# Kernel tuning notes

Hardware: AMD Instinct MI355X
Metric: run time of the kernel (lower is better)

## Reference

```python
import jax, jax.numpy as jnp
import numpy as np

# ---- fixed problem dimensions ----
B, S, T = 64, 200, 32          # batch of sequences, trees per seq, nodes per tree
V, E, C = 50000, 128, 128      # vocab, embedding_dim, encode_dim
H, OUT = 100, 104              # GRU hidden, output_dim
N = B * S * T                  # total nodes
D_MAX = 5                      # max depth of a 32-node complete binary tree


def setup_inputs() -> dict:
    key = jax.random.key(0)
    ks = jax.random.split(key, 16)
    # --- tree structure: every tree is a complete binary tree with T nodes ---
    local_parent = np.array([0] + [(i - 1) // 2 for i in range(1, T)], dtype=np.int64)
    local_depth = np.array([int(np.floor(np.log2(i + 1))) for i in range(T)], dtype=np.int64)
    num_trees = B * S
    offsets = np.arange(num_trees, dtype=np.int64) * T
    node_parent = (offsets[:, None] + local_parent[None, :]).reshape(-1)
    node_depth = np.tile(local_depth, num_trees)
    node_tree = np.repeat(np.arange(num_trees, dtype=np.int64), T)
    node_tokens = jax.random.randint(ks[0], (N,), 0, V, dtype=jnp.int64)
    sc = 0.05
    inp = {
        "node_tokens": node_tokens,
        "node_parent": jnp.asarray(node_parent),
        "node_tree": jnp.asarray(node_tree),
        "node_depth": jnp.asarray(node_depth),
        "emb": jax.random.normal(ks[1], (V, E), jnp.float32) * sc,
        "w_lin": jax.random.normal(ks[2], (C, E), jnp.float32) * sc,
        "b_lin": jnp.zeros((C,), jnp.float32),
        "w_ih_f": jax.random.normal(ks[3], (3 * H, C), jnp.float32) * sc,
        "w_hh_f": jax.random.normal(ks[4], (3 * H, H), jnp.float32) * sc,
        "b_ih_f": jnp.zeros((3 * H,), jnp.float32),
        "b_hh_f": jnp.zeros((3 * H,), jnp.float32),
        "w_ih_b": jax.random.normal(ks[5], (3 * H, C), jnp.float32) * sc,
        "w_hh_b": jax.random.normal(ks[6], (3 * H, H), jnp.float32) * sc,
        "b_ih_b": jnp.zeros((3 * H,), jnp.float32),
        "b_hh_b": jnp.zeros((3 * H,), jnp.float32),
        "fc_w": jax.random.normal(ks[7], (OUT, 2 * H), jnp.float32) * sc,
        "fc_b": jnp.zeros((OUT,), jnp.float32),
    }
    return inp


def _gru(x_sbc, w_ih, w_hh, b_ih, b_hh):
    """Torch-convention GRU over leading time axis. x_sbc: [S, B, C] -> [S, B, H]."""
    h0 = jnp.zeros((x_sbc.shape[1], w_hh.shape[1]), x_sbc.dtype)

    def step(h, xt):
        gx = xt @ w_ih.T + b_ih
        gh = h @ w_hh.T + b_hh
        xr, xz, xn = jnp.split(gx, 3, axis=-1)
        hr, hz, hn = jnp.split(gh, 3, axis=-1)
        r = jax.nn.sigmoid(xr + hr)
        z = jax.nn.sigmoid(xz + hz)
        n = jnp.tanh(xn + r * hn)
        h_new = (1.0 - z) * n + z * h
        return h_new, h_new

    _, hs = jax.lax.scan(step, h0, x_sbc)
    return hs


def reference(node_tokens, node_parent, node_tree, node_depth,
              emb, w_lin, b_lin,
              w_ih_f, w_hh_f, b_ih_f, b_hh_f,
              w_ih_b, w_hh_b, b_ih_b, b_hh_b,
              fc_w, fc_b):
    # per-node contribution: W * emb(token) + b   (recursion base of hidden_state)
    c = emb[node_tokens] @ w_lin.T + b_lin               # [N, C]
    # level-batched bottom-up scatter-add: h(node) = c(node) + sum(h(children))
    h = c
    for d in range(D_MAX, 0, -1):
        mask = (node_depth == d)[:, None]
        h = h.at[node_parent].add(jnp.where(mask, h, 0.0))
    # per-tree max pool over all node hidden states (TreeEncoder output)
    tree_vec = jax.ops.segment_max(h, node_tree, num_segments=B * S)  # [B*S, C]
    x = tree_vec.reshape(B, S, C)
    # bidirectional GRU (batch_first in torch; scan over time here)
    x_t = jnp.transpose(x, (1, 0, 2))                    # [S, B, C]
    fwd = _gru(x_t, w_ih_f, w_hh_f, b_ih_f, b_hh_f)      # [S, B, H]
    bwd = _gru(x_t[::-1], w_ih_b, w_hh_b, b_ih_b, b_hh_b)[::-1]
    gru_out = jnp.concatenate([fwd, bwd], axis=-1)       # [S, B, 2H]
    pool = gru_out.max(axis=0)                           # [B, 2H] (max over time)
    return pool @ fc_w.T + fc_b                          # [B, OUT]
```

## Files before the change

### kernel.cpp

```cpp
#include <hip/hip_runtime.h>
#include <hip/hip_bf16.h>
#include <math.h>

#define BB 64
#define SS 200
#define TT 32
#define EE 128
#define CC 128
#define HH 100
#define G3 300
#define OUTD 104
#define NTREE (BB*SS)
#define EMB_N (50000 * EE)

typedef __attribute__((ext_vector_type(4))) float f32x4;
typedef _Float16 f16x8 __attribute__((ext_vector_type(8)));

__device__ inline float fast_sigmoid(float x) {
    return __builtin_amdgcn_rcpf(1.f + __builtin_amdgcn_exp2f(-1.4426950408889634f * x));
}
__device__ inline float fast_tanh(float x) {
    return 1.f - 2.f * __builtin_amdgcn_rcpf(1.f + __builtin_amdgcn_exp2f(2.8853900817779268f * x));
}
__device__ inline unsigned pack2f16(float a, float b) {
    union { _Float16 h[2]; unsigned u; } x;
    x.h[0] = (_Float16)a; x.h[1] = (_Float16)b;
    return x.u;
}
__device__ inline unsigned f2u(float v) { union { float f; unsigned u; } x; x.f = v; return x.u; }
__device__ inline float u2f(unsigned v) { union { unsigned u; float f; } x; x.u = v; return x.f; }
__device__ inline float subtree_cnt(int p) {
    return (p == 0) ? 32.f : (p == 1) ? 16.f : (p == 2) ? 15.f :
           (p == 3) ? 8.f  : (p <= 6) ? 7.f  : (p == 7) ? 4.f  :
           (p <= 14) ? 3.f : (p == 15) ? 2.f : 1.f;
}

#define BAR() asm volatile("s_waitcnt lgkmcnt(0)\n\ts_barrier" ::: "memory")


__global__ __launch_bounds__(256) void k0_prep(const float* __restrict__ w_lin,
                                               const float* __restrict__ w_ih_f,
                                               const float* __restrict__ w_ih_b,
                                               const float* __restrict__ emb,
                                               _Float16* __restrict__ wl,
                                               _Float16* __restrict__ k2b,
                                               _Float16* __restrict__ lf,
                                               _Float16* __restrict__ emb16) {
    const int tid  = threadIdx.x;
    const int wave = tid >> 6;
    const int lane = tid & 63;
    const int r = lane & 15;
    const int q = lane >> 4;
    if (blockIdx.x == 0) {
#pragma unroll
        for (int nt = 0; nt < 2; ++nt)
#pragma unroll
            for (int kt = 0; kt < 4; ++kt) {
                const int n = wave * 32 + nt * 16 + r;
                const float* src = w_lin + (long)n * EE + kt * 32 + q * 8;
                f16x8 f;
#pragma unroll
                for (int e = 0; e < 8; ++e) f[e] = (_Float16)src[e];
                *(f16x8*)&wl[(size_t)((((wave * 2 + nt) * 4 + kt) * 64) + lane) * 8] = f;
            }
        if (wave == 0) {
#pragma unroll
            for (int mt2 = 0; mt2 < 2; ++mt2) {
                const int p = mt2 * 16 + r;
                f16x8 f;
#pragma unroll
                for (int e = 0; e < 8; ++e) {
                    int x = q * 8 + e;
                    while (x > p) x = (x - 1) >> 1;
                    f[e] = (_Float16)((x == p) ? 1.f : 0.f);
                }
                *(f16x8*)&lf[(size_t)(mt2 * 64 + lane) * 8] = f;
            }
        }
    } else if (blockIdx.x <= 10) {
        const int nb = blockIdx.x - 1;
        const int n = nb * 64 + wave * 16 + r;
        const int dir = (n >= 320) ? 1 : 0;
        const int j = n - dir * 320;
        const int jj = (j < G3) ? j : 0;
        const float* w = dir ? w_ih_b : w_ih_f;
#pragma unroll
        for (int kt = 0; kt < 4; ++kt) {
            const float* src = w + (long)jj * EE + kt * 32 + q * 8;
            f16x8 f;
#pragma unroll
            for (int e = 0; e < 8; ++e) f[e] = (_Float16)src[e];
            *(f16x8*)&k2b[(size_t)((((nb * 4 + wave) * 4 + kt) * 64) + lane) * 8] = f;
        }
    } else {
        const long base = (long)(blockIdx.x - 11) * 8192;
#pragma unroll
        for (int i = 0; i < 4; ++i) {
            const long off = base + i * 2048 + tid * 8;
            if (off < EMB_N) {
                const float4 e0 = ((const float4*)(emb + off))[0];
                const float4 e1 = ((const float4*)(emb + off))[1];
                f16x8 v;
                v[0] = (_Float16)e0.x; v[1] = (_Float16)e0.y; v[2] = (_Float16)e0.z; v[3] = (_Float16)e0.w;
                v[4] = (_Float16)e1.x; v[5] = (_Float16)e1.y; v[6] = (_Float16)e1.z; v[7] = (_Float16)e1.w;
                *(f16x8*)&emb16[off] = v;
            }
        }
    }
}

#define K1_TPB 4
#define K1_ROWS (K1_TPB * TT)
#define LDA 136
__global__ __launch_bounds__(512, 4) void k1_mfma(const int* __restrict__ tok,
                                                  const _Float16* __restrict__ emb16,
                                                  const _Float16* __restrict__ wl,
                                                  const _Float16* __restrict__ lf,
                                                  const float* __restrict__ b_lin,
                                                  _Float16* __restrict__ thi) {
    __shared__ __align__(16) _Float16 A_sh[K1_ROWS * LDA];
    __shared__ int tok_sh[K1_ROWS];

    const int tid  = threadIdx.x;
    const int wave = tid >> 6;
    const int lane = tid & 63;
    const int r = lane & 15;
    const int q = lane >> 4;

    f16x8 bfrag[4];
#pragma unroll
    for (int kt = 0; kt < 4; ++kt)
        bfrag[kt] = *(const f16x8*)&wl[(size_t)(((wave * 4 + kt) * 64) + lane) * 8];
    f16x8 l2f[2];
#pragma unroll
    for (int mt2 = 0; mt2 < 2; ++mt2)
        l2f[mt2] = *(const f16x8*)&lf[(size_t)(mt2 * 64 + lane) * 8];
    const float bias = b_lin[wave * 16 + r];

    const int tree0 = blockIdx.x * K1_TPB;
    if (tid < K1_ROWS) tok_sh[tid] = tok[tree0 * TT + tid];
    __syncthreads();

#pragma unroll
    for (int i = 0; i < 4; ++i) {
        const int idx = tid + i * 512;
        const int row = idx >> 4;
        const int p4  = idx & 15;
        f16x8 v = *(const f16x8*)&emb16[(size_t)tok_sh[row] * EE + p4 * 8];
        *(f16x8*)&A_sh[row * LDA + p4 * 8] = v;
    }
    __syncthreads();

    unsigned pk[8][2];
#pragma unroll
    for (int mt = 0; mt < 8; ++mt) {
        const int m = mt * 16 + r;
        f32x4 acc = (f32x4)(0.f);
#pragma unroll
        for (int kt = 0; kt < 4; ++kt) {
            f16x8 af = *(const f16x8*)&A_sh[m * LDA + kt * 32 + q * 8];
            acc = __builtin_amdgcn_mfma_f32_16x16x32_f16(af, bfrag[kt], acc, 0, 0, 0);
        }
        pk[mt][0] = pack2f16(acc[0], acc[1]);
        pk[mt][1] = pack2f16(acc[2], acc[3]);
    }

    const int l0 = (r + 16 * ((2 * q) & 3)) << 2;
    const int l1 = (r + 16 * ((2 * q + 1) & 3)) << 2;
    const bool hi = (q >> 1) != 0;
#pragma unroll
    for (int t = 0; t < K1_TPB; ++t) {
        const unsigned x0 = __builtin_amdgcn_ds_bpermute(l0, (int)pk[2 * t][0]);
        const unsigned y0 = __builtin_amdgcn_ds_bpermute(l0, (int)pk[2 * t + 1][0]);
        const unsigned x1 = __builtin_amdgcn_ds_bpermute(l0, (int)pk[2 * t][1]);
        const unsigned y1 = __builtin_amdgcn_ds_bpermute(l0, (int)pk[2 * t + 1][1]);
        const unsigned x2 = __builtin_amdgcn_ds_bpermute(l1, (int)pk[2 * t][0]);
        const unsigned y2 = __builtin_amdgcn_ds_bpermute(l1, (int)pk[2 * t + 1][0]);
        const unsigned x3 = __builtin_amdgcn_ds_bpermute(l1, (int)pk[2 * t][1]);
        const unsigned y3 = __builtin_amdgcn_ds_bpermute(l1, (int)pk[2 * t + 1][1]);
        union { unsigned u[4]; f16x8 v; } b2;
        b2.u[0] = hi ? y0 : x0;
        b2.u[1] = hi ? y1 : x1;
        b2.u[2] = hi ? y2 : x2;
        b2.u[3] = hi ? y3 : x3;

        float mx = -1e30f;
#pragma unroll
        for (int mt2 = 0; mt2 < 2; ++mt2) {
            f32x4 a2 = __builtin_amdgcn_mfma_f32_16x16x32_f16(l2f[mt2], b2.v, (f32x4)(0.f), 0, 0, 0);
#pragma unroll
            for (int reg = 0; reg < 4; ++reg) {
                const int p = mt2 * 16 + q * 4 + reg;
                mx = fmaxf(mx, a2[reg] + subtree_cnt(p) * bias);
            }
        }
        mx = fmaxf(mx, __shfl_xor(mx, 16, 64));
        mx = fmaxf(mx, __shfl_xor(mx, 32, 64));
        if (q == 0)
            thi[(size_t)(tree0 + t) * CC + wave * 16 + r] = (_Float16)mx;
    }
}

__global__ __launch_bounds__(256, 4) void k2_mfma(const _Float16* __restrict__ thi,
                                                  const _Float16* __restrict__ k2b,
                                                  const float* __restrict__ b_ih_f,
                                                  const float* __restrict__ b_ih_b,
                                                  float* __restrict__ gx) {
    __shared__ __align__(16) _Float16 Ah[128 * LDA];

    const int tid  = threadIdx.x;
    const int wave = tid >> 6;
    const int lane = tid & 63;
    const int r = lane & 15;
    const int q = lane >> 4;

    const int nb = blockIdx.x % 10;
    const int mb = blockIdx.x / 10;
    const int m0 = mb * 128;
    const int n0 = nb * 64;

#pragma unroll
    for (int i = 0; i < 8; ++i) {
        const int idx = tid + i * 256;
        const int row = idx >> 4;
        const int p   = idx & 15;
        f16x8 v = *(const f16x8*)&thi[(size_t)(m0 + row) * CC + p * 8];
        *(f16x8*)&Ah[row * LDA + p * 8] = v;
    }
    f16x8 bh[4];
#pragma unroll
    for (int kt = 0; kt < 4; ++kt)
        bh[kt] = *(const f16x8*)&k2b[(size_t)((((nb * 4 + wave) * 4 + kt) * 64) + lane) * 8];
    __syncthreads();

    const int ng  = n0 + wave * 16 + r;
    const int dir = (ng >= 320) ? 1 : 0;
    const int j   = ng - dir * 320;
    const bool valid = (j < G3);
    const float bias = valid ? (dir ? b_ih_b[j] : b_ih_f[j]) : 0.f;
    float* gxd = gx + (long)dir * NTREE * G3;

#pragma unroll
    for (int mt = 0; mt < 8; ++mt) {
        const int m = mt * 16 + r;
        f32x4 acc = (f32x4)(0.f);
#pragma unroll
        for (int kt = 0; kt < 4; ++kt) {
            f16x8 a = *(const f16x8*)&Ah[m * LDA + kt * 32 + q * 8];
            acc = __builtin_amdgcn_mfma_f32_16x16x32_f16(a, bh[kt], acc, 0, 0, 0);
        }
        if (valid) {
#pragma unroll
            for (int reg = 0; reg < 4; ++reg) {
                const int mm = m0 + mt * 16 + q * 4 + reg;
                gxd[(long)mm * G3 + j] = acc[reg] + bias;
            }
        }
    }
}

__global__ __launch_bounds__(256, 1) void k3_gru(const float* __restrict__ gx,
                                                 const float* __restrict__ w_hh_f,
                                                 const float* __restrict__ b_hh_f,
                                                 const float* __restrict__ w_hh_b,
                                                 const float* __restrict__ b_hh_b,
                                                 float* __restrict__ pool) {
    const int bid = blockIdx.x;
    const int dir = bid & 1;
    const int b = bid >> 1;
    const float* w_hh = dir ? w_hh_b : w_hh_f;
    const float* b_hh = dir ? b_hh_b : b_hh_f;

    __shared__ __align__(16) _Float16 h_sh[2][128];

    const int tid  = threadIdx.x;
    const int wave = tid >> 6;
    const int lane = tid & 63;
    const int r = lane & 15;
    const int q = lane >> 4;

    f16x8 bf[5][4];
#pragma unroll
    for (int i = 0; i < 5; ++i) {
        const int l = i * 16 + r;
        const int gate = l / 25;
        const int ch   = l - gate * 25;
        const bool nv  = (l < 75);
        const int row  = gate * HH + wave * 25 + ch;
#pragma unroll
        for (int kt = 0; kt < 4; ++kt) {
            f16x8 f;
#pragma unroll
            for (int e = 0; e < 8; ++e) {
                const int k = kt * 32 + q * 8 + e;
                f[e] = (_Float16)((nv && k < HH) ? w_hh[row * HH + k] : 0.f);
            }
            bf[i][kt] = f;
        }
    }

    const int m = lane;
    const int c = wave * 25 + m;
    const bool act = (m < 25);
    float br = 0.f, bz = 0.f, bn = 0.f;
    if (act) { br = b_hh[c]; bz = b_hh[HH + c]; bn = b_hh[2 * HH + c]; }

    if (tid < 128) { h_sh[0][tid] = (_Float16)0.f; h_sh[1][tid] = (_Float16)0.f; }

    const float* gxd = gx + (long)dir * NTREE * G3;
    const int sstep = dir ? -1 : 1;
    int s = dir ? (SS - 1) : 0;
    float xr = 0.f, xz = 0.f, xn = 0.f;
    if (act) {
        const float* row0 = gxd + ((long)b * SS + s) * G3;
        xr = row0[c]; xz = row0[HH + c]; xn = row0[2 * HH + c];
    }
    float hj = 0.f, hmax = -1e30f;
    const int lz = ((25 + m) & 15) << 2;
    const int ln = ((50 + m) & 15) << 2;
    __syncthreads();

    for (int t = 0; t < SS; ++t) {
        const int p = t & 1;
        const int s_n = s + sstep;
        float xrn = 0.f, xzn = 0.f, xnn = 0.f;
        if (act && t < SS - 1) {
            const float* row0 = gxd + ((long)b * SS + s_n) * G3;
            xrn = row0[c]; xzn = row0[HH + c]; xnn = row0[2 * HH + c];
        }

        f16x8 a[4];
#pragma unroll
        for (int kt = 0; kt < 4; ++kt)
            a[kt] = *(const f16x8*)&h_sh[p][kt * 32 + q * 8];
        float g[5];
#pragma unroll
        for (int i = 0; i < 5; ++i) {
            f32x4 a0 = __builtin_amdgcn_mfma_f32_16x16x32_f16(a[0], bf[i][0], (f32x4)(0.f), 0, 0, 0);
            a0       = __builtin_amdgcn_mfma_f32_16x16x32_f16(a[1], bf[i][1], a0, 0, 0, 0);
            f32x4 a1 = __builtin_amdgcn_mfma_f32_16x16x32_f16(a[2], bf[i][2], (f32x4)(0.f), 0, 0, 0);
            a1       = __builtin_amdgcn_mfma_f32_16x16x32_f16(a[3], bf[i][3], a1, 0, 0, 0);
            g[i] = a0[0] + a1[0];
        }

        const unsigned bz1 = __builtin_amdgcn_ds_bpermute(lz, (int)f2u(g[1]));
        const unsigned bz2 = __builtin_amdgcn_ds_bpermute(lz, (int)f2u(g[2]));
        const unsigned bz3 = __builtin_amdgcn_ds_bpermute(lz, (int)f2u(g[3]));
        const unsigned bn3 = __builtin_amdgcn_ds_bpermute(ln, (int)f2u(g[3]));
        const unsigned bn4 = __builtin_amdgcn_ds_bpermute(ln, (int)f2u(g[4]));

        if (act) {
            const float ghr = (m < 16) ? g[0] : g[1];
            const float ghz = (m < 7) ? u2f(bz1) : (m < 23) ? u2f(bz2) : u2f(bz3);
            const float ghn = (m < 14) ? u2f(bn3) : u2f(bn4);
            const float rg = fast_sigmoid(xr + ghr + br);
            const float zg = fast_sigmoid(xz + ghz + bz);
            const float ng = fast_tanh(xn + rg * (ghn + bn));
            hj = (1.f - zg) * ng + zg * hj;
            hmax = fmaxf(hmax, hj);
            h_sh[1 - p][c] = (_Float16)hj;
            xr = xrn; xz = xzn; xn = xnn;
        }
        BAR();
        s = s_n;
    }
    if (act) pool[(long)b * (2 * HH) + dir * HH + c] = hmax;
}

__global__ __launch_bounds__(256) void k4_fc(const float* __restrict__ pool,
                                             const float* __restrict__ fc_w,
                                             const float* __restrict__ fc_b,
                                             float* __restrict__ out) {
    const int b = blockIdx.x;
    __shared__ __align__(16) float p_sh[2 * HH];
    const int t = threadIdx.x;
    if (t < 2 * HH) p_sh[t] = pool[(long)b * (2 * HH) + t];
    __syncthreads();
    if (t < OUTD) {
        const float4* wr4 = (const float4*)(fc_w + (long)t * (2 * HH));
        const float4* p4 = (const float4*)p_sh;
        float a0 = 0.f, a1 = 0.f;
#pragma unroll
        for (int k = 0; k < 50; k += 2) {
            float4 w0 = wr4[k],   p0 = p4[k];
            float4 w1 = wr4[k+1], p1 = p4[k+1];
            a0 += w0.x*p0.x + w0.y*p0.y + w0.z*p0.z + w0.w*p0.w;
            a1 += w1.x*p1.x + w1.y*p1.y + w1.z*p1.z + w1.w*p1.w;
        }
        out[(long)b * OUTD + t] = fc_b[t] + a0 + a1;
    }
}

extern "C" void kernel_launch(void* const* d_in, const int* in_sizes, int n_in,
                              void* d_out, int out_size, void* d_ws, size_t ws_size,
                              hipStream_t stream) {
    const int*   tok    = (const int*)d_in[0];
    const float* emb    = (const float*)d_in[4];
    const float* w_lin  = (const float*)d_in[5];
    const float* b_lin  = (const float*)d_in[6];
    const float* w_ih_f = (const float*)d_in[7];
    const float* w_hh_f = (const float*)d_in[8];
    const float* b_ih_f = (const float*)d_in[9];
    const float* b_hh_f = (const float*)d_in[10];
    const float* w_ih_b = (const float*)d_in[11];
    const float* w_hh_b = (const float*)d_in[12];
    const float* b_ih_b = (const float*)d_in[13];
    const float* b_hh_b = (const float*)d_in[14];
    const float* fc_w   = (const float*)d_in[15];
    const float* fc_b   = (const float*)d_in[16];

    char* wsb = (char*)d_ws;
    _Float16* wl    = (_Float16*)(wsb);
    _Float16* k2b   = (_Float16*)(wsb + 32768);
    _Float16* lf    = (_Float16*)(wsb + 196608);
    _Float16* thi   = (_Float16*)(wsb + 198656);
    float*    gx    = (float*)(wsb + 3475456);
    _Float16* emb16 = (_Float16*)(wsb + 3475456);
    float*    pool  = (float*)(wsb);
    float*    out   = (float*)d_out;

    k0_prep<<<11 + 782, 256, 0, stream>>>(w_lin, w_ih_f, w_ih_b, emb, wl, k2b, lf, emb16);
    k1_mfma<<<NTREE / K1_TPB, 512, 0, stream>>>(tok, emb16, wl, lf, b_lin, thi);
    k2_mfma<<<(NTREE / 128) * 10, 256, 0, stream>>>(thi, k2b, b_ih_f, b_ih_b, gx);
    k3_gru <<<2 * BB, 256, 0, stream>>>(gx, w_hh_f, b_hh_f, w_hh_b, b_hh_b, pool);
    k4_fc  <<<BB, 256, 0, stream>>>(pool, fc_w, fc_b, out);
}
```

Baseline: 247.6 us.

## Fuse input-gate GEMM into tree encoder and gather fp32 embeddings directly

Removes the full-table fp32-to-fp16 conversion of the embedding matrix, so only the rows actually gathered are read from fp32 and converted in-kernel. Fuses the GRU input projection into the tree-encoder kernel: each block keeps its 4 tree vectors in shared memory and runs the 640-column MFMA against k2b, writing gx directly. This drops the thi intermediate and a kernel launch. In exchange, each of the 3200 blocks re-reads the whole k2b weight from L2, the gathers move twice as many bytes per row, and MFMA tiles are mostly padding because only 4 of 16 rows are valid.

```diff
diff --git a/kernel.cpp b/kernel.cpp
--- a/kernel.cpp
+++ b/kernel.cpp
@@ -11,7 +11,6 @@
 #define G3 300
 #define OUTD 104
 #define NTREE (BB*SS)
-#define EMB_N (50000 * EE)
 
 typedef __attribute__((ext_vector_type(4))) float f32x4;
 typedef _Float16 f16x8 __attribute__((ext_vector_type(8)));
@@ -41,11 +40,9 @@
 __global__ __launch_bounds__(256) void k0_prep(const float* __restrict__ w_lin,
                                                const float* __restrict__ w_ih_f,
                                                const float* __restrict__ w_ih_b,
-                                               const float* __restrict__ emb,
                                                _Float16* __restrict__ wl,
                                                _Float16* __restrict__ k2b,
-                                               _Float16* __restrict__ lf,
-                                               _Float16* __restrict__ emb16) {
+                                               _Float16* __restrict__ lf) {
     const int tid  = threadIdx.x;
     const int wave = tid >> 6;
     const int lane = tid & 63;
@@ -77,7 +74,7 @@
                 *(f16x8*)&lf[(size_t)(mt2 * 64 + lane) * 8] = f;
             }
         }
-    } else if (blockIdx.x <= 10) {
+    } else {
         const int nb = blockIdx.x - 1;
         const int n = nb * 64 + wave * 16 + r;
         const int dir = (n >= 320) ? 1 : 0;
@@ -92,33 +89,23 @@
             for (int e = 0; e < 8; ++e) f[e] = (_Float16)src[e];
             *(f16x8*)&k2b[(size_t)((((nb * 4 + wave) * 4 + kt) * 64) + lane) * 8] = f;
         }
-    } else {
-        const long base = (long)(blockIdx.x - 11) * 8192;
-#pragma unroll
-        for (int i = 0; i < 4; ++i) {
-            const long off = base + i * 2048 + tid * 8;
-            if (off < EMB_N) {
-                const float4 e0 = ((const float4*)(emb + off))[0];
-                const float4 e1 = ((const float4*)(emb + off))[1];
-                f16x8 v;
-                v[0] = (_Float16)e0.x; v[1] = (_Float16)e0.y; v[2] = (_Float16)e0.z; v[3] = (_Float16)e0.w;
-                v[4] = (_Float16)e1.x; v[5] = (_Float16)e1.y; v[6] = (_Float16)e1.z; v[7] = (_Float16)e1.w;
-                *(f16x8*)&emb16[off] = v;
-            }
-        }
     }
 }
 
 #define K1_TPB 4
 #define K1_ROWS (K1_TPB * TT)
 #define LDA 136
-__global__ __launch_bounds__(512, 4) void k1_mfma(const int* __restrict__ tok,
-                                                  const _Float16* __restrict__ emb16,
-                                                  const _Float16* __restrict__ wl,
-                                                  const _Float16* __restrict__ lf,
-                                                  const float* __restrict__ b_lin,
-                                                  _Float16* __restrict__ thi) {
+__global__ __launch_bounds__(512, 4) void k1_fused(const int* __restrict__ tok,
+                                                   const float* __restrict__ emb,
+                                                   const _Float16* __restrict__ wl,
+                                                   const _Float16* __restrict__ k2b,
+                                                   const _Float16* __restrict__ lf,
+                                                   const float* __restrict__ b_lin,
+                                                   const float* __restrict__ b_ih_f,
+                                                   const float* __restrict__ b_ih_b,
+                                                   float* __restrict__ gx) {
     __shared__ __align__(16) _Float16 A_sh[K1_ROWS * LDA];
+    __shared__ __align__(16) _Float16 x_sh[16 * LDA];
     __shared__ int tok_sh[K1_ROWS];
 
     const int tid  = threadIdx.x;
@@ -139,6 +126,7 @@
 
     const int tree0 = blockIdx.x * K1_TPB;
     if (tid < K1_ROWS) tok_sh[tid] = tok[tree0 * TT + tid];
+    for (int i = tid; i < 16 * LDA; i += 512) x_sh[i] = (_Float16)0.f;
     __syncthreads();
 
 #pragma unroll
@@ -146,7 +134,11 @@
         const int idx = tid + i * 512;
         const int row = idx >> 4;
         const int p4  = idx & 15;
-        f16x8 v = *(const f16x8*)&emb16[(size_t)tok_sh[row] * EE + p4 * 8];
+        const float4* src = (const float4*)(emb + (long)tok_sh[row] * EE + p4 * 8);
+        const float4 e0 = src[0], e1 = src[1];
+        f16x8 v;
+        v[0] = (_Float16)e0.x; v[1] = (_Float16)e0.y; v[2] = (_Float16)e0.z; v[3] = (_Float16)e0.w;
+        v[4] = (_Float16)e1.x; v[5] = (_Float16)e1.y; v[6] = (_Float16)e1.z; v[7] = (_Float16)e1.w;
         *(f16x8*)&A_sh[row * LDA + p4 * 8] = v;
     }
     __syncthreads();
@@ -197,64 +189,33 @@
         mx = fmaxf(mx, __shfl_xor(mx, 16, 64));
         mx = fmaxf(mx, __shfl_xor(mx, 32, 64));
         if (q == 0)
-            thi[(size_t)(tree0 + t) * CC + wave * 16 + r] = (_Float16)mx;
-    }
-}
-
-__global__ __launch_bounds__(256, 4) void k2_mfma(const _Float16* __restrict__ thi,
-                                                  const _Float16* __restrict__ k2b,
-                                                  const float* __restrict__ b_ih_f,
-                                                  const float* __restrict__ b_ih_b,
-                                                  float* __restrict__ gx) {
-    __shared__ __align__(16) _Float16 Ah[128 * LDA];
-
-    const int tid  = threadIdx.x;
-    const int wave = tid >> 6;
-    const int lane = tid & 63;
-    const int r = lane & 15;
-    const int q = lane >> 4;
-
-    const int nb = blockIdx.x % 10;
-    const int mb = blockIdx.x / 10;
-    const int m0 = mb * 128;
-    const int n0 = nb * 64;
-
-#pragma unroll
-    for (int i = 0; i < 8; ++i) {
-        const int idx = tid + i * 256;
-        const int row = idx >> 4;
-        const int p   = idx & 15;
-        f16x8 v = *(const f16x8*)&thi[(size_t)(m0 + row) * CC + p * 8];
-        *(f16x8*)&Ah[row * LDA + p * 8] = v;
-    }
-    f16x8 bh[4];
+            x_sh[t * LDA + wave * 16 + r] = (_Float16)mx;
+    }
+    __syncthreads();
+
+    f16x8 a2f[4];
 #pragma unroll
     for (int kt = 0; kt < 4; ++kt)
-        bh[kt] = *(const f16x8*)&k2b[(size_t)((((nb * 4 + wave) * 4 + kt) * 64) + lane) * 8];
-    __syncthreads();
-
-    const int ng  = n0 + wave * 16 + r;
-    const int dir = (ng >= 320) ? 1 : 0;
-    const int j   = ng - dir * 320;
-    const bool valid = (j < G3);
-    const float bias = valid ? (dir ? b_ih_b[j] : b_ih_f[j]) : 0.f;
-    float* gxd = gx + (long)dir * NTREE * G3;
-
-#pragma unroll
-    for (int mt = 0; mt < 8; ++mt) {
-        const int m = mt * 16 + r;
+        a2f[kt] = *(const f16x8*)&x_sh[r * LDA + kt * 32 + q * 8];
+
+#pragma unroll
+    for (int i = 0; i < 5; ++i) {
+        const int ntg = wave * 5 + i;
         f32x4 acc = (f32x4)(0.f);
 #pragma unroll
         for (int kt = 0; kt < 4; ++kt) {
-            f16x8 a = *(const f16x8*)&Ah[m * LDA + kt * 32 + q * 8];
-            acc = __builtin_amdgcn_mfma_f32_16x16x32_f16(a, bh[kt], acc, 0, 0, 0);
-        }
-        if (valid) {
-#pragma unroll
-            for (int reg = 0; reg < 4; ++reg) {
-                const int mm = m0 + mt * 16 + q * 4 + reg;
-                gxd[(long)mm * G3 + j] = acc[reg] + bias;
-            }
+            const f16x8 bh = *(const f16x8*)&k2b[(size_t)(((ntg * 4 + kt) * 64) + lane) * 8];
+            acc = __builtin_amdgcn_mfma_f32_16x16x32_f16(a2f[kt], bh, acc, 0, 0, 0);
+        }
+        const int ng  = ntg * 16 + r;
+        const int dir = (ng >= 320) ? 1 : 0;
+        const int j   = ng - dir * 320;
+        if (q == 0 && j < G3) {
+            const float bih = dir ? b_ih_b[j] : b_ih_f[j];
+            float* gxd = gx + (long)dir * NTREE * G3;
+#pragma unroll
+            for (int reg = 0; reg < 4; ++reg)
+                gxd[(long)(tree0 + reg) * G3 + j] = acc[reg] + bih;
         }
     }
 }
@@ -410,18 +371,16 @@
     const float* fc_b   = (const float*)d_in[16];
 
     char* wsb = (char*)d_ws;
-    _Float16* wl    = (_Float16*)(wsb);
-    _Float16* k2b   = (_Float16*)(wsb + 32768);
-    _Float16* lf    = (_Float16*)(wsb + 196608);
-    _Float16* thi   = (_Float16*)(wsb + 198656);
-    float*    gx    = (float*)(wsb + 3475456);
-    _Float16* emb16 = (_Float16*)(wsb + 3475456);
-    float*    pool  = (float*)(wsb);
-    float*    out   = (float*)d_out;
-
-    k0_prep<<<11 + 782, 256, 0, stream>>>(w_lin, w_ih_f, w_ih_b, emb, wl, k2b, lf, emb16);
-    k1_mfma<<<NTREE / K1_TPB, 512, 0, stream>>>(tok, emb16, wl, lf, b_lin, thi);
-    k2_mfma<<<(NTREE / 128) * 10, 256, 0, stream>>>(thi, k2b, b_ih_f, b_ih_b, gx);
+    _Float16* wl   = (_Float16*)(wsb);
+    _Float16* k2b  = (_Float16*)(wsb + 32768);
+    _Float16* lf   = (_Float16*)(wsb + 196608);
+    float*    gx   = (float*)(wsb + 198656);
+    float*    pool = (float*)(wsb);
+    float*    out  = (float*)d_out;
+
+    k0_prep<<<11, 256, 0, stream>>>(w_lin, w_ih_f, w_ih_b, wl, k2b, lf);
+    k1_fused<<<NTREE / K1_TPB, 512, 0, stream>>>(tok, emb, wl, k2b, lf, b_lin,
+                                                 b_ih_f, b_ih_b, gx);
     k3_gru <<<2 * BB, 256, 0, stream>>>(gx, w_hh_f, b_hh_f, w_hh_b, b_hh_b, pool);
     k4_fc  <<<BB, 256, 0, stream>>>(pool, fc_w, fc_b, out);
 }
```

Result: slower. 254.3 us (+2.7%).
